# Kernel optimization log

Hardware: AMD Instinct MI355X
Metric: run time of the kernel (lower is better)

## Reference

```python
import jax, jax.numpy as jnp
import numpy as np

B, S, D, H, FF = 4, 1024, 1024, 16, 4096
DH = D // H
EPS = 1e-5


def setup_inputs() -> dict:
    key = jax.random.key(0)
    ks = jax.random.split(key, 24)
    w = lambda i, shp: jax.random.normal(ks[i], shp, jnp.float32) * 0.02
    inp = {
        'tgt': jax.random.normal(ks[0], (B, S, D), jnp.float32),
        'memory': jax.random.normal(ks[1], (B, S, D), jnp.float32),
        'mask': jax.random.randint(ks[2], (B, S, S), 0, 2, jnp.int32),
        # self-attention projections (stored [in,out]; torch Linear weight transposed)
        'sa_wq': w(3, (D, D)), 'sa_bq': jnp.zeros((D,), jnp.float32),
        'sa_wk': w(4, (D, D)), 'sa_bk': jnp.zeros((D,), jnp.float32),
        'sa_wv': w(5, (D, D)), 'sa_bv': jnp.zeros((D,), jnp.float32),
        'sa_wo': w(6, (D, D)), 'sa_bo': jnp.zeros((D,), jnp.float32),
        # cross-attention projections
        'ca_wq': w(7, (D, D)), 'ca_bq': jnp.zeros((D,), jnp.float32),
        'ca_wk': w(8, (D, D)), 'ca_bk': jnp.zeros((D,), jnp.float32),
        'ca_wv': w(9, (D, D)), 'ca_bv': jnp.zeros((D,), jnp.float32),
        'ca_wo': w(10, (D, D)), 'ca_bo': jnp.zeros((D,), jnp.float32),
        # FFN
        'w1': w(11, (D, FF)), 'b1': jnp.zeros((FF,), jnp.float32),
        'w2': w(12, (FF, D)), 'b2': jnp.zeros((D,), jnp.float32),
        # LayerNorms
        'g1': jnp.ones((D,), jnp.float32), 'be1': jnp.zeros((D,), jnp.float32),
        'g2': jnp.ones((D,), jnp.float32), 'be2': jnp.zeros((D,), jnp.float32),
        'g3': jnp.ones((D,), jnp.float32), 'be3': jnp.zeros((D,), jnp.float32),
    }
    return inp


def _layernorm(x, g, b):
    m = jnp.mean(x, axis=-1, keepdims=True)
    v = jnp.mean((x - m) ** 2, axis=-1, keepdims=True)
    return (x - m) * jax.lax.rsqrt(v + EPS) * g + b


def _mha(x, y, mask, wq, bq, wk, bk, wv, bv, wo, bo):
    # chunk(h,-1)+cat(0) head-split == reshape to [B,S,H,DH]
    b_, sq, _ = x.shape
    sk = y.shape[1]
    q = (x @ wq + bq).reshape(b_, sq, H, DH)
    k = (y @ wk + bk).reshape(b_, sk, H, DH)
    v = (y @ wv + bv).reshape(b_, sk, H, DH)
    score = jnp.einsum('bqhd,bkhd->bhqk', q, k) / jnp.float32(np.sqrt(DH))
    score = score + (1.0 - mask[:, None].astype(score.dtype)) * (-1e9)
    attn = jax.nn.softmax(score, axis=-1)
    out = jnp.einsum('bhqk,bkhd->bqhd', attn, v).reshape(b_, sq, D)
    return out @ wo + bo


def reference(tgt, memory, mask,
              sa_wq, sa_bq, sa_wk, sa_bk, sa_wv, sa_bv, sa_wo, sa_bo,
              ca_wq, ca_bq, ca_wk, ca_bk, ca_wv, ca_bv, ca_wo, ca_bo,
              w1, b1, w2, b2, g1, be1, g2, be2, g3, be3):
    t = tgt + _mha(tgt, tgt, mask, sa_wq, sa_bq, sa_wk, sa_bk, sa_wv, sa_bv, sa_wo, sa_bo)
    t = _layernorm(t, g1, be1)
    t = t + _mha(t, memory, mask, ca_wq, ca_bq, ca_wk, ca_bk, ca_wv, ca_bv, ca_wo, ca_bo)
    t = _layernorm(t, g2, be2)
    t = t + (jax.nn.relu(t @ w1 + b1) @ w2 + b2)
    t = _layernorm(t, g3, be3)
    return t
```

## Files before the change

kernel.cpp:

```cpp
#include <hip/hip_runtime.h>
#include <math.h>

typedef float f32x4 __attribute__((ext_vector_type(4)));
typedef unsigned short ushort8 __attribute__((ext_vector_type(8)));
typedef unsigned short ushort4v __attribute__((ext_vector_type(4)));
typedef __bf16 bf16x8 __attribute__((ext_vector_type(8)));
typedef unsigned int u32;

__device__ __forceinline__ unsigned short f2bf(float x) {
  union { float f; unsigned u; } v; v.f = x;
  unsigned r = v.u + 0x7FFFu + ((v.u >> 16) & 1u);
  return (unsigned short)(r >> 16);
}
__device__ __forceinline__ float bf2f(unsigned short u) {
  union { unsigned u; float f; } c; c.u = ((unsigned)u) << 16; return c.f;
}

__device__ __forceinline__ f32x4 mfma16(ushort8 a, ushort8 b, f32x4 c) {
  return __builtin_amdgcn_mfma_f32_16x16x32_bf16(
      __builtin_bit_cast(bf16x8, a), __builtin_bit_cast(bf16x8, b), c, 0, 0, 0);
}

__device__ __forceinline__ void gload16(const void* g, void* l) {
  __builtin_amdgcn_global_load_lds((const __attribute__((address_space(1))) u32*)g,
                                   (__attribute__((address_space(3))) u32*)l, 16, 0, 0);
}

__device__ __forceinline__ int xcd_swz(int orig, int nwg) {
  int q = nwg >> 3, r = nwg & 7;
  int xcd = orig & 7, lid = orig >> 3;
  return (xcd < r ? xcd * (q + 1) : r * (q + 1) + (xcd - r) * q) + lid;
}

__global__ __launch_bounds__(256) void gemm_bf16_kernel(
    const unsigned short* __restrict__ A, const unsigned short* __restrict__ Bt,
    const float* __restrict__ bias, void* __restrict__ C,
    int M, int N, int K, int flags)
{
  __shared__ __align__(16) char As0[128 * 128];
  __shared__ __align__(16) char Bs0[128 * 128];
  __shared__ __align__(16) char As1[128 * 128];
  __shared__ __align__(16) char Bs1[128 * 128];
  const int gx = gridDim.x;
  const int wg = xcd_swz(blockIdx.x + gx * blockIdx.y, gx * gridDim.y);
  const int bn = wg % gx, bm = wg / gx;
  const int t = threadIdx.x;
  const int lane = t & 63, w = t >> 6, wm = w >> 1, wn = w & 1;
  const int l4 = lane & 15, lg = lane >> 4;
  const size_t K2 = (size_t)K * 2;

  f32x4 acc[4][4];
#pragma unroll
  for (int i = 0; i < 4; ++i)
#pragma unroll
    for (int j = 0; j < 4; ++j) acc[i][j] = f32x4{0.f, 0.f, 0.f, 0.f};

  const int lr = lane >> 3;
  const int ls = (lane & 7) ^ lr;
  const char* Ag = (const char*)A + (size_t)(bm * 128 + w * 32 + lr) * K2 + ls * 16;
  const char* Bg = (const char*)Bt + (size_t)(bn * 128 + w * 32 + lr) * K2 + ls * 16;
  const int wo = w * 4096;

  auto STAGE = [&](char* Al, char* Bl, int kt) {
    const size_t ko = (size_t)kt * 128;
#pragma unroll
    for (int i = 0; i < 4; ++i) {
      gload16(Ag + i * 8 * K2 + ko, Al + wo + i * 1024);
      gload16(Bg + i * 8 * K2 + ko, Bl + wo + i * 1024);
    }
  };
  auto COMPUTE = [&](const char* As, const char* Bs) {
#pragma unroll
    for (int ks = 0; ks < 2; ++ks) {
      const int kb = ks * 64 + lg * 16;
      ushort8 af[4], bfr[4];
#pragma unroll
      for (int mi = 0; mi < 4; ++mi) {
        int r = wm * 64 + mi * 16 + l4;
        af[mi] = *reinterpret_cast<const ushort8*>(As + r * 128 + (kb ^ ((r & 7) << 4)));
      }
#pragma unroll
      for (int ni = 0; ni < 4; ++ni) {
        int r = wn * 64 + ni * 16 + l4;
        bfr[ni] = *reinterpret_cast<const ushort8*>(Bs + r * 128 + (kb ^ ((r & 7) << 4)));
      }
#pragma unroll
      for (int mi = 0; mi < 4; ++mi)
#pragma unroll
        for (int ni = 0; ni < 4; ++ni)
          acc[mi][ni] = mfma16(af[mi], bfr[ni], acc[mi][ni]);
    }
  };

#define GWAIT(more) do { if (more) asm volatile("s_waitcnt vmcnt(8)" ::: "memory"); \
                         else      asm volatile("s_waitcnt vmcnt(0)" ::: "memory"); } while (0)

  const int nkt = K >> 6;
  STAGE(As0, Bs0, 0);
  STAGE(As1, Bs1, 1);
  for (int kt = 0; kt < nkt; kt += 2) {
    GWAIT(kt + 1 < nkt);
    __builtin_amdgcn_s_barrier();
    __builtin_amdgcn_sched_barrier(0);
    COMPUTE(As0, Bs0);
    __builtin_amdgcn_s_barrier();
    __builtin_amdgcn_sched_barrier(0);
    if (kt + 2 < nkt) STAGE(As0, Bs0, kt + 2);
    GWAIT(kt + 2 < nkt);
    __builtin_amdgcn_s_barrier();
    __builtin_amdgcn_sched_barrier(0);
    COMPUTE(As1, Bs1);
    __builtin_amdgcn_s_barrier();
    __builtin_amdgcn_sched_barrier(0);
    if (kt + 3 < nkt) STAGE(As1, Bs1, kt + 3);
  }
#undef GWAIT

  const int relu = flags & 1, obf = flags & 2;
#pragma unroll
  for (int mi = 0; mi < 4; ++mi)
#pragma unroll
    for (int ni = 0; ni < 4; ++ni) {
      int col = bn * 128 + wn * 64 + ni * 16 + l4;
      float bia = bias[col];
#pragma unroll
      for (int j = 0; j < 4; ++j) {
        int row = bm * 128 + wm * 64 + mi * 16 + lg * 4 + j;
        float vv = acc[mi][ni][j] + bia;
        if (relu) vv = fmaxf(vv, 0.f);
        if (obf) ((unsigned short*)C)[(size_t)row * N + col] = f2bf(vv);
        else     ((float*)C)[(size_t)row * N + col] = vv;
      }
    }
}

constexpr int kS = 1024, kD = 1024, kDH = 64;

__global__ __launch_bounds__(256) void attn_kernel(
    const unsigned short* __restrict__ Qg, const unsigned short* __restrict__ Kg,
    const unsigned short* __restrict__ Vg, int qs, int ks_,
    const unsigned short* __restrict__ mpack, unsigned short* __restrict__ Og)
{
  __shared__ __align__(16) char Ks0[8192];
  __shared__ __align__(16) char Ks1[8192];
  __shared__ __align__(16) char VT0[8192];
  __shared__ __align__(16) char VT1[8192];
  __shared__ __align__(16) char Ps[8192];
  const int wg = xcd_swz(blockIdx.x + 16 * (blockIdx.y + 16 * blockIdx.z), 1024);
  const int qt = wg & 15, h = (wg >> 4) & 15, b = wg >> 8;
  const int t = threadIdx.x, lane = t & 63, w = t >> 6;
  const int l4 = lane & 15, lg = lane >> 4;
  const int lr = lane >> 3, sg = (lane & 7) ^ lr;

  ushort8 q0, q1;
  {
    const unsigned short* src = Qg + (size_t)(b * kS + qt * 64 + w * 16 + l4) * qs + h * kDH;
    q0 = *reinterpret_cast<const ushort8*>(src + lg * 8);
    q1 = *reinterpret_cast<const ushort8*>(src + 32 + lg * 8);
  }
  const unsigned short* mtb = mpack + (size_t)(b * 16 + qt) * 4096 + t;

  auto stageK = [&](char* Kl, int kt) {
    const char* base = (const char*)(Kg + (size_t)(b * kS + kt * 64) * ks_ + h * kDH) + sg * 16;
    gload16(base + (size_t)(w * 16 + lr) * (ks_ * 2), Kl + w * 2048);
    gload16(base + (size_t)(w * 16 + 8 + lr) * (ks_ * 2), Kl + w * 2048 + 1024);
  };

  float m_r[4], l_p[4];
  f32x4 o[4];
#pragma unroll
  for (int j = 0; j < 4; ++j) { m_r[j] = -1e30f; l_p[j] = 0.f; }
#pragma unroll
  for (int di = 0; di < 4; ++di) o[di] = f32x4{0.f, 0.f, 0.f, 0.f};

  ushort8 vA0, vA1, vB0, vB1;
  unsigned short mA, mB;
  stageK(Ks0, 0);
  {
    const unsigned short* vsrc = Vg + (size_t)(b * kS + (t >> 2)) * ks_ + h * kDH + (t & 3) * 16;
    vA0 = *reinterpret_cast<const ushort8*>(vsrc);
    vA1 = *reinterpret_cast<const ushort8*>(vsrc + 8);
    mA = mtb[0];
  }

#define ATTN_TILE(KC, VC, KN, VC0, VC1, VN0, VN1, MCUR, MNXT, KTV)                       \
  {                                                                                      \
    asm volatile("s_waitcnt vmcnt(0)" ::: "memory");                                     \
    {       \
      int key2 = (t >> 2) * 2, c0 = (t & 3) * 16;                                        \
      _Pragma("unroll")                                                                  \
      for (int i = 0; i < 8; ++i) {                                                      \
        int dh = c0 + i;                                                                 \
        *(unsigned short*)(VC + dh * 128 +                                               \
            (key2 ^ ((dh & 7) << 4) ^ ((dh >> 4) << 5))) = VC0[i];                       \
      }                                                                                  \
      _Pragma("unroll")                                                                  \
      for (int i = 0; i < 8; ++i) {                                                      \
        int dh = c0 + 8 + i;                                                             \
        *(unsigned short*)(VC + dh * 128 +                                               \
            (key2 ^ ((dh & 7) << 4) ^ ((dh >> 4) << 5))) = VC1[i];                       \
      }                                                                                  \
    }                                                                                    \
    asm volatile("s_waitcnt lgkmcnt(0)" ::: "memory");                                   \
    __builtin_amdgcn_s_barrier();                                                        \
    __builtin_amdgcn_sched_barrier(0);                                                   \
    if ((KTV) + 1 < 16) {                  \
      stageK(KN, (KTV) + 1);                                                             \
      const unsigned short* vsrc = Vg +                                                  \
          (size_t)(b * kS + ((KTV) + 1) * 64 + (t >> 2)) * ks_ + h * kDH + (t & 3) * 16; \
      VN0 = *reinterpret_cast<const ushort8*>(vsrc);                                     \
      VN1 = *reinterpret_cast<const ushort8*>(vsrc + 8);                                 \
      MNXT = mtb[((KTV) + 1) * 256];                                                     \
    }                                                                                    \
    f32x4 sc[4];                                                                         \
    _Pragma("unroll")                                                                    \
    for (int ni = 0; ni < 4; ++ni) sc[ni] = f32x4{0.f, 0.f, 0.f, 0.f};                   \
    __builtin_amdgcn_s_setprio(1);                                                       \
    _Pragma("unroll")                                                                    \
    for (int ks = 0; ks < 2; ++ks) {                                                     \
      const int kb = ks * 64 + lg * 16;                                                  \
      ushort8 a = ks ? q1 : q0;                                                          \
      _Pragma("unroll")                                                                  \
      for (int ni = 0; ni < 4; ++ni) {                                                   \
        int kr = ni * 16 + l4;                                                           \
        ushort8 bb = *(const ushort8*)(KC + kr * 128 + (kb ^ ((kr & 7) << 4)));          \
        sc[ni] = mfma16(a, bb, sc[ni]);                                                  \
      }                                                                                  \
    }                                                                                    \
    __builtin_amdgcn_s_setprio(0);                                                       \
    const unsigned mbits_ = (unsigned)(MCUR);                                            \
    float tmax[4];                                                                       \
    _Pragma("unroll")                                                                    \
    for (int j = 0; j < 4; ++j) {                                                        \
      _Pragma("unroll")                                                                  \
      for (int ni = 0; ni < 4; ++ni)                                                     \
        if (!((mbits_ >> (ni * 4 + j)) & 1u)) sc[ni][j] = -1e9f;                         \
      tmax[j] = fmaxf(fmaxf(sc[0][j], sc[1][j]), fmaxf(sc[2][j], sc[3][j]));             \
    }                                                                                    \
    bool need = (tmax[0] > m_r[0] + 8.f) || (tmax[1] > m_r[1] + 8.f) ||                  \
                (tmax[2] > m_r[2] + 8.f) || (tmax[3] > m_r[3] + 8.f);                    \
    if (__any(need)) {                 \
      _Pragma("unroll")                                                                  \
      for (int j = 0; j < 4; ++j) {                                                      \
        tmax[j] = fmaxf(tmax[j], __shfl_xor(tmax[j], 1, 64));                            \
        tmax[j] = fmaxf(tmax[j], __shfl_xor(tmax[j], 2, 64));                            \
        tmax[j] = fmaxf(tmax[j], __shfl_xor(tmax[j], 4, 64));                            \
        tmax[j] = fmaxf(tmax[j], __shfl_xor(tmax[j], 8, 64));                            \
        float mn = fmaxf(m_r[j], tmax[j]);                                               \
        float al = exp2f(m_r[j] - mn);                                                   \
        m_r[j] = mn; l_p[j] *= al;                                                       \
        o[0][j] *= al; o[1][j] *= al; o[2][j] *= al; o[3][j] *= al;                      \
      }                                                                                  \
    }                                                                                    \
    _Pragma("unroll")                                                                    \
    for (int ni = 0; ni < 4; ++ni)                                                       \
      _Pragma("unroll")                                                                  \
      for (int j = 0; j < 4; ++j) {                                                      \
        float p = exp2f(sc[ni][j] - m_r[j]);                                             \
        sc[ni][j] = p;                                                                   \
        l_p[j] += p;                                                                     \
      }                                                                                  \
    {                               \
      char* Pw = Ps + w * 2048;                                                          \
      _Pragma("unroll")                                                                  \
      for (int ni = 0; ni < 4; ++ni)                                                     \
        _Pragma("unroll")                                                                \
        for (int j = 0; j < 4; ++j) {                                                    \
          int row = lg * 4 + j, col = ni * 16 + l4;                                      \
          *(unsigned short*)(Pw + row * 128 +                                            \
              ((col * 2) ^ ((row & 7) << 4) ^ ((row & 8) << 2))) =                       \
              __builtin_bit_cast(unsigned short, (__bf16)sc[ni][j]);                     \
        }                                                                                \
    }                                                                                    \
    asm volatile("s_waitcnt lgkmcnt(0)" ::: "memory");                                   \
    __builtin_amdgcn_sched_barrier(0);                                                   \
    __builtin_amdgcn_s_setprio(1);                                                       \
    {                      \
      const char* Pw = Ps + w * 2048;                                                    \
      _Pragma("unroll")                                                                  \
      for (int ks = 0; ks < 2; ++ks) {                                                   \
        const int kb = ks * 64 + lg * 16;                                                \
        ushort8 pa = *(const ushort8*)(Pw + l4 * 128 +                                   \
            (kb ^ ((l4 & 7) << 4) ^ ((l4 & 8) << 2)));                                   \
        _Pragma("unroll")                                                                \
        for (int di = 0; di < 4; ++di) {                                                 \
          int vr2 = di * 16 + l4;                                                        \
          ushort8 vb = *(const ushort8*)(VC + vr2 * 128 +                                \
              (kb ^ ((vr2 & 7) << 4) ^ ((vr2 >> 4) << 5)));                              \
          o[di] = mfma16(pa, vb, o[di]);                                                 \
        }                                                                                \
      }                                                                                  \
    }                                                                                    \
    __builtin_amdgcn_s_setprio(0);                                                       \
  }

  for (int kt = 0; kt < 16; kt += 2) {
    ATTN_TILE(Ks0, VT0, Ks1, vA0, vA1, vB0, vB1, mA, mB, kt);
    ATTN_TILE(Ks1, VT1, Ks0, vB0, vB1, vA0, vA1, mB, mA, kt + 1);
  }
#undef ATTN_TILE

  float rinv[4];
#pragma unroll
  for (int j = 0; j < 4; ++j) {
    float s = l_p[j];
    s += __shfl_xor(s, 1, 64);
    s += __shfl_xor(s, 2, 64);
    s += __shfl_xor(s, 4, 64);
    s += __shfl_xor(s, 8, 64);
    rinv[j] = 1.0f / s;
  }
#pragma unroll
  for (int di = 0; di < 4; ++di) {
    int col = h * kDH + di * 16 + l4;
#pragma unroll
    for (int j = 0; j < 4; ++j) {
      int qrow = qt * 64 + w * 16 + lg * 4 + j;
      Og[(size_t)(b * kS + qrow) * kD + col] =
          __builtin_bit_cast(unsigned short, (__bf16)(o[di][j] * rinv[j]));
    }
  }
}

__global__ __launch_bounds__(256) void addln_kernel(
    const float* __restrict__ x, const unsigned short* __restrict__ y,
    const float* __restrict__ g, const float* __restrict__ be,
    float* __restrict__ out, unsigned short* __restrict__ ob)
{
  const int row = blockIdx.x, t = threadIdx.x;
  const size_t base = (size_t)row * 1024 + t * 4;
  float4 xv = *reinterpret_cast<const float4*>(x + base);
  ushort4v yv = *reinterpret_cast<const ushort4v*>(y + base);
  float v0 = xv.x + bf2f(yv[0]), v1 = xv.y + bf2f(yv[1]);
  float v2 = xv.z + bf2f(yv[2]), v3 = xv.w + bf2f(yv[3]);
  float s1 = v0 + v1 + v2 + v3;
  float s2 = v0 * v0 + v1 * v1 + v2 * v2 + v3 * v3;
#pragma unroll
  for (int off = 1; off < 64; off <<= 1) {
    s1 += __shfl_xor(s1, off, 64);
    s2 += __shfl_xor(s2, off, 64);
  }
  __shared__ float r1[4], r2[4];
  const int w = t >> 6, lane = t & 63;
  if (lane == 0) { r1[w] = s1; r2[w] = s2; }
  __syncthreads();
  s1 = r1[0] + r1[1] + r1[2] + r1[3];
  s2 = r2[0] + r2[1] + r2[2] + r2[3];
  const float mean = s1 * (1.0f / 1024.0f);
  const float var = s2 * (1.0f / 1024.0f) - mean * mean;
  const float rs = rsqrtf(var + 1e-5f);
  float4 gv = *reinterpret_cast<const float4*>(g + t * 4);
  float4 bv = *reinterpret_cast<const float4*>(be + t * 4);
  float4 ov;
  ov.x = (v0 - mean) * rs * gv.x + bv.x;
  ov.y = (v1 - mean) * rs * gv.y + bv.y;
  ov.z = (v2 - mean) * rs * gv.z + bv.z;
  ov.w = (v3 - mean) * rs * gv.w + bv.w;
  *reinterpret_cast<float4*>(out + base) = ov;
  if (ob) {
    ushort4v bo;
    bo[0] = f2bf(ov.x); bo[1] = f2bf(ov.y); bo[2] = f2bf(ov.z); bo[3] = f2bf(ov.w);
    *reinterpret_cast<ushort4v*>(ob + base) = bo;
  }
}

__global__ __launch_bounds__(256) void cvt2_bf16_kernel(
    const float* __restrict__ a, const float* __restrict__ b,
    unsigned short* __restrict__ da, unsigned short* __restrict__ db, int n8each)
{
  int i = blockIdx.x * 256 + threadIdx.x;
  const float* s = a; unsigned short* d = da;
  if (i >= n8each) { s = b; d = db; i -= n8each; }
  if (i >= n8each) return;
  float4 f0 = reinterpret_cast<const float4*>(s)[i * 2];
  float4 f1 = reinterpret_cast<const float4*>(s)[i * 2 + 1];
  ushort8 v;
  v[0] = f2bf(f0.x); v[1] = f2bf(f0.y); v[2] = f2bf(f0.z); v[3] = f2bf(f0.w);
  v[4] = f2bf(f1.x); v[5] = f2bf(f1.y); v[6] = f2bf(f1.z); v[7] = f2bf(f1.w);
  reinterpret_cast<ushort8*>(d)[i] = v;
}

__global__ __launch_bounds__(256) void transpose_cvt_kernel(
    const float* __restrict__ src, unsigned short* __restrict__ dst, int K, int N)
{
  __shared__ float tile[32][33];
  const int bx = blockIdx.x, by = blockIdx.y;
  const int tx = threadIdx.x & 31, ty = threadIdx.x >> 5;
#pragma unroll
  for (int i = 0; i < 4; ++i)
    tile[ty + i * 8][tx] = src[(size_t)(by * 32 + ty + i * 8) * N + bx * 32 + tx];
  __syncthreads();
#pragma unroll
  for (int i = 0; i < 4; ++i)
    dst[(size_t)(bx * 32 + ty + i * 8) * K + by * 32 + tx] = f2bf(tile[tx][ty + i * 8]);
}

struct TPtrs { const float* s[8]; unsigned short* d[8]; float scale[8]; };
__global__ __launch_bounds__(256) void tcvt_batch_kernel(TPtrs p)
{
  __shared__ float tile[32][33];
  const float* __restrict__ src = p.s[blockIdx.z];
  unsigned short* __restrict__ dst = p.d[blockIdx.z];
  const float sc = p.scale[blockIdx.z];
  const int bx = blockIdx.x, by = blockIdx.y;
  const int tx = threadIdx.x & 31, ty = threadIdx.x >> 5;
#pragma unroll
  for (int i = 0; i < 4; ++i)
    tile[ty + i * 8][tx] = src[(size_t)(by * 32 + ty + i * 8) * 1024 + bx * 32 + tx];
  __syncthreads();
#pragma unroll
  for (int i = 0; i < 4; ++i)
    dst[(size_t)(bx * 32 + ty + i * 8) * 1024 + by * 32 + tx] = f2bf(tile[tx][ty + i * 8] * sc);
}

__global__ void biasprep_kernel(const float* sq, const float* sk, const float* sv,
                                const float* cq, const float* ck, const float* cv,
                                float* bsa, float* bca, float* bcq, float s)
{
  int i = blockIdx.x * 256 + threadIdx.x;
  if (i < 1024) { bsa[i] = sq[i] * s; bcq[i] = cq[i] * s; bca[i] = ck[i]; bca[i + 1024] = cv[i]; }
  else if (i < 2048) bsa[i] = sk[i - 1024];
  else if (i < 3072) bsa[i] = sv[i - 2048];
}

__global__ __launch_bounds__(256) void maskprep_kernel(
    const int* __restrict__ mask, unsigned short* __restrict__ mpack)
{
  int idx = blockIdx.x * 256 + threadIdx.x;
  int t = idx & 255;
  int kt = (idx >> 8) & 15;
  int qt = (idx >> 12) & 15;
  int b = idx >> 16;
  int qb = qt * 64 + ((t >> 6) & 3) * 16 + ((t >> 4) & 3) * 4;
  int kb = kt * 64 + (t & 15);
  unsigned m = 0;
#pragma unroll
  for (int ni = 0; ni < 4; ++ni)
#pragma unroll
    for (int j = 0; j < 4; ++j)
      if (mask[(size_t)(b * 1024 + qb + j) * 1024 + kb + ni * 16]) m |= 1u << (ni * 4 + j);
  mpack[idx] = (unsigned short)m;
}

extern "C" void kernel_launch(void* const* d_in, const int* in_sizes, int n_in,
                              void* d_out, int out_size, void* d_ws, size_t ws_size,
                              hipStream_t stream)
{
  const float* tgt  = (const float*)d_in[0];
  const float* memi = (const float*)d_in[1];
  const int*   mask = (const int*)d_in[2];
  const float* sa_wq = (const float*)d_in[3];  const float* sa_bq = (const float*)d_in[4];
  const float* sa_wk = (const float*)d_in[5];  const float* sa_bk = (const float*)d_in[6];
  const float* sa_wv = (const float*)d_in[7];  const float* sa_bv = (const float*)d_in[8];
  const float* sa_wo = (const float*)d_in[9];  const float* sa_bo = (const float*)d_in[10];
  const float* ca_wq = (const float*)d_in[11]; const float* ca_bq = (const float*)d_in[12];
  const float* ca_wk = (const float*)d_in[13]; const float* ca_bk = (const float*)d_in[14];
  const float* ca_wv = (const float*)d_in[15]; const float* ca_bv = (const float*)d_in[16];
  const float* ca_wo = (const float*)d_in[17]; const float* ca_bo = (const float*)d_in[18];
  const float* w1 = (const float*)d_in[19]; const float* b1 = (const float*)d_in[20];
  const float* w2 = (const float*)d_in[21]; const float* b2 = (const float*)d_in[22];
  const float* g1 = (const float*)d_in[23]; const float* be1 = (const float*)d_in[24];
  const float* g2 = (const float*)d_in[25]; const float* be2 = (const float*)d_in[26];
  const float* g3 = (const float*)d_in[27]; const float* be3 = (const float*)d_in[28];
  float* out = (float*)d_out;
  char* W = (char*)d_ws;
  const size_t MB = 1 << 20;
  typedef unsigned short us;
  const float QSCALE = 0.18033688011112042f;

  us* Wsaqkv = (us*)(W + 0);
  us* Wsao   = (us*)(W + 6 * MB);
  us* Wcaq   = (us*)(W + 8 * MB);
  us* Wcakv  = (us*)(W + 10 * MB);
  us* Wcao   = (us*)(W + 14 * MB);
  us* W1t    = (us*)(W + 16 * MB);
  us* W2t    = (us*)(W + 24 * MB);
  float* b_saqkv = (float*)(W + 32 * MB);
  float* b_cakv  = (float*)(W + 32 * MB + 16384);
  float* b_caq   = (float*)(W + 32 * MB + 32768);
  us* tgt_bf = (us*)(W + 33 * MB);
  us* T2b    = tgt_bf;
  us* mem_bf = (us*)(W + 41 * MB);
  us* QKV    = (us*)(W + 49 * MB);
  us* Qca    = (us*)(W + 49 * MB);
  us* KVca   = (us*)(W + 57 * MB);
  us* T1b    = (us*)(W + 65 * MB);
  us* AO     = (us*)(W + 73 * MB);
  us* Hb     = (us*)(W + 49 * MB);
  us* Opb    = (us*)(W + 81 * MB);
  us* mpack  = (us*)(W + 89 * MB);
  float* T1f = (float*)(W + 98 * MB);
  float* T2f = T1f;

  const int M = 4096;
  dim3 blk(256);
  auto gemm = [&](const us* Aa, const us* Bta, const float* bias, void* Cc,
                  int Nn, int Kk, int flags) {
    gemm_bf16_kernel<<<dim3(Nn / 128, M / 128), blk, 0, stream>>>(Aa, Bta, bias, Cc, M, Nn, Kk, flags);
  };

  TPtrs tp;
  tp.s[0] = sa_wq; tp.d[0] = Wsaqkv;              tp.scale[0] = QSCALE;
  tp.s[1] = sa_wk; tp.d[1] = Wsaqkv + 1024 * 1024; tp.scale[1] = 1.f;
  tp.s[2] = sa_wv; tp.d[2] = Wsaqkv + 2048 * 1024; tp.scale[2] = 1.f;
  tp.s[3] = sa_wo; tp.d[3] = Wsao;                 tp.scale[3] = 1.f;
  tp.s[4] = ca_wq; tp.d[4] = Wcaq;                 tp.scale[4] = QSCALE;
  tp.s[5] = ca_wk; tp.d[5] = Wcakv;                tp.scale[5] = 1.f;
  tp.s[6] = ca_wv; tp.d[6] = Wcakv + 1024 * 1024;  tp.scale[6] = 1.f;
  tp.s[7] = ca_wo; tp.d[7] = Wcao;                 tp.scale[7] = 1.f;
  tcvt_batch_kernel<<<dim3(32, 32, 8), blk, 0, stream>>>(tp);
  transpose_cvt_kernel<<<dim3(128, 32), blk, 0, stream>>>(w1, W1t, 1024, 4096);
  transpose_cvt_kernel<<<dim3(32, 128), blk, 0, stream>>>(w2, W2t, 4096, 1024);
  cvt2_bf16_kernel<<<dim3(4096), blk, 0, stream>>>(tgt, memi, tgt_bf, mem_bf, M * 1024 / 8);
  biasprep_kernel<<<dim3(12), blk, 0, stream>>>(sa_bq, sa_bk, sa_bv, ca_bq, ca_bk, ca_bv,
                                                b_saqkv, b_cakv, b_caq, QSCALE);
  maskprep_kernel<<<dim3(1024), blk, 0, stream>>>(mask, mpack);

  gemm(tgt_bf, Wsaqkv, b_saqkv, QKV, 3072, 1024, 2);
  attn_kernel<<<dim3(16, 16, 4), blk, 0, stream>>>(QKV, QKV + 1024, QKV + 2048, 3072, 3072, mpack, AO);
  gemm(AO, Wsao, sa_bo, Opb, 1024, 1024, 2);
  addln_kernel<<<dim3(M), blk, 0, stream>>>(tgt, Opb, g1, be1, T1f, T1b);

  gemm(T1b, Wcaq, b_caq, Qca, 1024, 1024, 2);
  gemm(mem_bf, Wcakv, b_cakv, KVca, 2048, 1024, 2);
  attn_kernel<<<dim3(16, 16, 4), blk, 0, stream>>>(Qca, KVca, KVca + 1024, 1024, 2048, mpack, AO);
  gemm(AO, Wcao, ca_bo, Opb, 1024, 1024, 2);
  addln_kernel<<<dim3(M), blk, 0, stream>>>(T1f, Opb, g2, be2, T2f, T2b);

  gemm(T2b, W1t, b1, Hb, 4096, 1024, 3);
  gemm(Hb, W2t, b2, Opb, 1024, 4096, 2);
  addln_kernel<<<dim3(M), blk, 0, stream>>>(T2f, Opb, g3, be3, out, nullptr);

  (void)in_sizes; (void)n_in; (void)out_size; (void)ws_size;
}
```

Baseline: 399.4 us.

## Split K in two for N=1024 GEMMs and sum partials in add-LayerNorm

```diff
diff --git a/kernel.cpp b/kernel.cpp
--- a/kernel.cpp
+++ b/kernel.cpp
@@ -44,6 +44,7 @@
   const int gx = gridDim.x;
   const int wg = xcd_swz(blockIdx.x + gx * blockIdx.y, gx * gridDim.y);
   const int bn = wg % gx, bm = wg / gx;
+  const int z = blockIdx.z;
   const int t = threadIdx.x;
   const int lane = t & 63, w = t >> 6, wm = w >> 1, wn = w & 1;
   const int l4 = lane & 15, lg = lane >> 4;
@@ -95,24 +96,25 @@
 #define GWAIT(more) do { if (more) asm volatile("s_waitcnt vmcnt(8)" ::: "memory"); \
                          else      asm volatile("s_waitcnt vmcnt(0)" ::: "memory"); } while (0)
 
-  const int nkt = K >> 6;
-  STAGE(As0, Bs0, 0);
-  STAGE(As1, Bs1, 1);
-  for (int kt = 0; kt < nkt; kt += 2) {
-    GWAIT(kt + 1 < nkt);
+  const int nkt2 = (K >> 6) / gridDim.z;
+  const int kbeg = z * nkt2, kend = kbeg + nkt2;
+  STAGE(As0, Bs0, kbeg);
+  STAGE(As1, Bs1, kbeg + 1);
+  for (int kt = kbeg; kt < kend; kt += 2) {
+    GWAIT(kt + 1 < kend);
     __builtin_amdgcn_s_barrier();
     __builtin_amdgcn_sched_barrier(0);
     COMPUTE(As0, Bs0);
     __builtin_amdgcn_s_barrier();
     __builtin_amdgcn_sched_barrier(0);
-    if (kt + 2 < nkt) STAGE(As0, Bs0, kt + 2);
-    GWAIT(kt + 2 < nkt);
+    if (kt + 2 < kend) STAGE(As0, Bs0, kt + 2);
+    GWAIT(kt + 2 < kend);
     __builtin_amdgcn_s_barrier();
     __builtin_amdgcn_sched_barrier(0);
     COMPUTE(As1, Bs1);
     __builtin_amdgcn_s_barrier();
     __builtin_amdgcn_sched_barrier(0);
-    if (kt + 3 < nkt) STAGE(As1, Bs1, kt + 3);
+    if (kt + 3 < kend) STAGE(As1, Bs1, kt + 3);
   }
 #undef GWAIT
 
@@ -122,14 +124,15 @@
 #pragma unroll
     for (int ni = 0; ni < 4; ++ni) {
       int col = bn * 128 + wn * 64 + ni * 16 + l4;
-      float bia = bias[col];
+      float bia = (z == 0) ? bias[col] : 0.f;
 #pragma unroll
       for (int j = 0; j < 4; ++j) {
         int row = bm * 128 + wm * 64 + mi * 16 + lg * 4 + j;
         float vv = acc[mi][ni][j] + bia;
         if (relu) vv = fmaxf(vv, 0.f);
-        if (obf) ((unsigned short*)C)[(size_t)row * N + col] = f2bf(vv);
-        else     ((float*)C)[(size_t)row * N + col] = vv;
+        size_t idx = (size_t)z * M * N + (size_t)row * N + col;
+        if (obf) ((unsigned short*)C)[idx] = f2bf(vv);
+        else     ((float*)C)[idx] = vv;
       }
     }
 }
@@ -323,16 +326,20 @@
 }
 
 __global__ __launch_bounds__(256) void addln_kernel(
-    const float* __restrict__ x, const unsigned short* __restrict__ y,
+    const float* __restrict__ x, const unsigned short* __restrict__ y0,
+    const unsigned short* __restrict__ y1,
     const float* __restrict__ g, const float* __restrict__ be,
     float* __restrict__ out, unsigned short* __restrict__ ob)
 {
   const int row = blockIdx.x, t = threadIdx.x;
   const size_t base = (size_t)row * 1024 + t * 4;
   float4 xv = *reinterpret_cast<const float4*>(x + base);
-  ushort4v yv = *reinterpret_cast<const ushort4v*>(y + base);
-  float v0 = xv.x + bf2f(yv[0]), v1 = xv.y + bf2f(yv[1]);
-  float v2 = xv.z + bf2f(yv[2]), v3 = xv.w + bf2f(yv[3]);
+  ushort4v yv0 = *reinterpret_cast<const ushort4v*>(y0 + base);
+  ushort4v yv1 = *reinterpret_cast<const ushort4v*>(y1 + base);
+  float v0 = xv.x + bf2f(yv0[0]) + bf2f(yv1[0]);
+  float v1 = xv.y + bf2f(yv0[1]) + bf2f(yv1[1]);
+  float v2 = xv.z + bf2f(yv0[2]) + bf2f(yv1[2]);
+  float v3 = xv.w + bf2f(yv0[3]) + bf2f(yv1[3]);
   float s1 = v0 + v1 + v2 + v3;
   float s2 = v0 * v0 + v1 * v1 + v2 * v2 + v3 * v3;
 #pragma unroll
@@ -442,6 +449,11 @@
   mpack[idx] = (unsigned short)m;
 }
 
+__global__ void zfill_kernel(unsigned short* dst, int n8) {
+  int i = blockIdx.x * 256 + threadIdx.x;
+  if (i < n8) reinterpret_cast<ushort8*>(dst)[i] = ushort8{0,0,0,0,0,0,0,0};
+}
+
 extern "C" void kernel_launch(void* const* d_in, const int* in_sizes, int n_in,
                               void* d_out, int out_size, void* d_ws, size_t ws_size,
                               hipStream_t stream)
@@ -488,15 +500,17 @@
   us* AO     = (us*)(W + 73 * MB);
   us* Hb     = (us*)(W + 49 * MB);
   us* Opb    = (us*)(W + 81 * MB);
-  us* mpack  = (us*)(W + 89 * MB);
+  us* mpack  = (us*)(W + 97 * MB);
   float* T1f = (float*)(W + 98 * MB);
   float* T2f = T1f;
+  us* Opb1   = Opb + 4096 * 1024;
 
   const int M = 4096;
   dim3 blk(256);
   auto gemm = [&](const us* Aa, const us* Bta, const float* bias, void* Cc,
-                  int Nn, int Kk, int flags) {
-    gemm_bf16_kernel<<<dim3(Nn / 128, M / 128), blk, 0, stream>>>(Aa, Bta, bias, Cc, M, Nn, Kk, flags);
+                  int Nn, int Kk, int flags, int zsplit) {
+    gemm_bf16_kernel<<<dim3(Nn / 128, M / 128, zsplit), blk, 0, stream>>>(
+        Aa, Bta, bias, Cc, M, Nn, Kk, flags);
   };
 
   TPtrs tp;
@@ -516,20 +530,20 @@
                                                 b_saqkv, b_cakv, b_caq, QSCALE);
   maskprep_kernel<<<dim3(1024), blk, 0, stream>>>(mask, mpack);
 
-  gemm(tgt_bf, Wsaqkv, b_saqkv, QKV, 3072, 1024, 2);
+  gemm(tgt_bf, Wsaqkv, b_saqkv, QKV, 3072, 1024, 2, 1);
   attn_kernel<<<dim3(16, 16, 4), blk, 0, stream>>>(QKV, QKV + 1024, QKV + 2048, 3072, 3072, mpack, AO);
-  gemm(AO, Wsao, sa_bo, Opb, 1024, 1024, 2);
-  addln_kernel<<<dim3(M), blk, 0, stream>>>(tgt, Opb, g1, be1, T1f, T1b);
-
-  gemm(T1b, Wcaq, b_caq, Qca, 1024, 1024, 2);
-  gemm(mem_bf, Wcakv, b_cakv, KVca, 2048, 1024, 2);
+  gemm(AO, Wsao, sa_bo, Opb, 1024, 1024, 2, 2);
+  addln_kernel<<<dim3(M), blk, 0, stream>>>(tgt, Opb, Opb1, g1, be1, T1f, T1b);
+
+  gemm(T1b, Wcaq, b_caq, Qca, 1024, 1024, 2, 1);
+  gemm(mem_bf, Wcakv, b_cakv, KVca, 2048, 1024, 2, 1);
   attn_kernel<<<dim3(16, 16, 4), blk, 0, stream>>>(Qca, KVca, KVca + 1024, 1024, 2048, mpack, AO);
-  gemm(AO, Wcao, ca_bo, Opb, 1024, 1024, 2);
-  addln_kernel<<<dim3(M), blk, 0, stream>>>(T1f, Opb, g2, be2, T2f, T2b);
-
-  gemm(T2b, W1t, b1, Hb, 4096, 1024, 3);
-  gemm(Hb, W2t, b2, Opb, 1024, 4096, 2);
-  addln_kernel<<<dim3(M), blk, 0, stream>>>(T2f, Opb, g3, be3, out, nullptr);
+  gemm(AO, Wcao, ca_bo, Opb, 1024, 1024, 2, 2);
+  addln_kernel<<<dim3(M), blk, 0, stream>>>(T1f, Opb, Opb1, g2, be2, T2f, T2b);
+
+  gemm(T2b, W1t, b1, Hb, 4096, 1024, 3, 1);
+  gemm(Hb, W2t, b2, Opb, 1024, 4096, 2, 2);
+  addln_kernel<<<dim3(M), blk, 0, stream>>>(T2f, Opb, Opb1, g3, be3, out, nullptr);
 
   (void)in_sizes; (void)n_in; (void)out_size; (void)ws_size;
 }
```

Result: no change. 398.1 us (-0.3%).
